# Kernel tuning notes

Measured on AMD Instinct MI355X. Metric: run time of the kernel, lower is better.

The kernel has to match this reference:

```python
import jax, jax.numpy as jnp
import numpy as np

NUM_HEADS = 8


def _conv1x1(x, W, b):
    # 1x1 conv == per-pixel linear: x [N,C,H,W], W [O,C], b [O]
    return jnp.einsum('nchw,oc->nohw', x, W) + b[None, :, None, None]


def setup_inputs() -> dict:
    key = jax.random.key(0)
    ks = jax.random.split(key, 10)
    C = 512
    s = 1.0 / np.sqrt(C)  # keep pre-softmax logits in a sane range
    return {
        'x': jax.random.normal(ks[0], (2, C, 64, 64), dtype=jnp.float32),
        'Wq': jax.random.normal(ks[1], (C, C), dtype=jnp.float32) * s,
        'bq': jax.random.normal(ks[2], (C,), dtype=jnp.float32) * 0.01,
        'Wk': jax.random.normal(ks[3], (C, C), dtype=jnp.float32) * s,
        'bk': jax.random.normal(ks[4], (C,), dtype=jnp.float32) * 0.01,
        'Wv': jax.random.normal(ks[5], (C, C), dtype=jnp.float32) * s,
        'bv': jax.random.normal(ks[6], (C,), dtype=jnp.float32) * 0.01,
        'Wo': jax.random.normal(ks[7], (C, C), dtype=jnp.float32) * s,
        'bo': jax.random.normal(ks[8], (C,), dtype=jnp.float32) * 0.01,
        'gamma': jax.random.normal(ks[9], (1,), dtype=jnp.float32),
    }


def reference(x, Wq, bq, Wk, bk, Wv, bv, Wo, bo, gamma):
    N, C, H, W = x.shape
    nh = NUM_HEADS
    hd = C // nh
    S = H * W
    scale = 1.0 / (hd ** 0.5)
    # Projections via 1x1 conv, then split heads over flattened spatial tokens
    Q = _conv1x1(x, Wq, bq).reshape(N, nh, hd, S).transpose(0, 1, 3, 2)  # [N,h,S,d]
    K = _conv1x1(x, Wk, bk).reshape(N, nh, hd, S)                         # [N,h,d,S]
    V = _conv1x1(x, Wv, bv).reshape(N, nh, hd, S).transpose(0, 1, 3, 2)  # [N,h,S,d]
    attn = jax.nn.softmax(jnp.einsum('nhsd,nhdt->nhst', Q, K) * scale, axis=-1)
    out = jnp.einsum('nhst,nhtd->nhsd', attn, V)                          # [N,h,S,d]
    out = out.transpose(0, 1, 3, 2).reshape(N, C, H, W)
    out = _conv1x1(out, Wo, bo)
    return gamma[0] * out + x
```

## Files before the change

### kernel.cpp

```cpp
#include <hip/hip_runtime.h>
#include <hip/hip_bf16.h>

typedef __attribute__((ext_vector_type(4))) float f32x4;
typedef __attribute__((ext_vector_type(16))) float f32x16;
typedef __attribute__((ext_vector_type(8))) short s16x8;
typedef __attribute__((ext_vector_type(4))) unsigned short us16x4;
typedef __attribute__((ext_vector_type(4))) unsigned int u32x4;

#define C_DIM 512
#define S_DIM 4096
#define NB 2
#define NH 8
#define HD 64

#define QSCALE 0.1803368801111244f

__device__ __forceinline__ unsigned short f2bf(float f) {
    union { float f; unsigned u; } v; v.f = f;
    unsigned r = v.u + 0x7FFFu + ((v.u >> 16) & 1u);
    return (unsigned short)(r >> 16);
}

__device__ __forceinline__ float dev_exp2(float x) {
    float r;
    asm("v_exp_f32 %0, %1" : "=v"(r) : "v"(x));
    return r;
}

__device__ __forceinline__ unsigned cvt_pk_bf16(float lo, float hi) {
    unsigned r;
    asm("v_cvt_pk_bf16_f32 %0, %1, %2" : "=v"(r) : "v"(lo), "v"(hi));
    return r;
}

__device__ __forceinline__ void lane_swap(unsigned& a, unsigned& b) {
    asm("v_permlane32_swap_b32 %0, %1" : "+v"(a), "+v"(b));
}

__global__ __launch_bounds__(256) void wconv_kernel(
    const float* __restrict__ Wq, const float* __restrict__ Wk,
    const float* __restrict__ Wv, const float* __restrict__ Wo,
    unsigned short* __restrict__ Wb) {
    int i = blockIdx.x * 256 + threadIdx.x;
    int y = blockIdx.y;
    const float* src = (y == 0) ? Wq : (y == 1) ? Wk : (y == 2) ? Wv : Wo;
    Wb[(size_t)y * 262144 + i] = f2bf(src[i]);
}

__global__ __launch_bounds__(256) void xpose_kernel(
    const float* __restrict__ x, unsigned short* __restrict__ Xt) {
    __shared__ float tile[32][33];
    int n = blockIdx.z;
    int s0 = blockIdx.x * 32;
    int c0 = blockIdx.y * 32;
    int tx = threadIdx.x & 31;
    int ty = threadIdx.x >> 5;
#pragma unroll
    for (int r = 0; r < 4; ++r) {
        int c = c0 + ty + r * 8;
        tile[ty + r * 8][tx] = x[((size_t)n * C_DIM + c) * S_DIM + s0 + tx];
    }
    __syncthreads();
#pragma unroll
    for (int r = 0; r < 4; ++r) {
        int s = s0 + ty + r * 8;
        Xt[((size_t)n * S_DIM + s) * C_DIM + c0 + tx] = f2bf(tile[tx][ty + r * 8]);
    }
}

__global__ __launch_bounds__(256) void qkv_gemm_kernel(
    const unsigned short* __restrict__ Wb, const unsigned short* __restrict__ Xt,
    const float* __restrict__ bq, const float* __restrict__ bk, const float* __restrict__ bv,
    unsigned short* __restrict__ Qt, unsigned short* __restrict__ Kt,
    unsigned short* __restrict__ Vb) {
    __shared__ unsigned short As[128 * 72];
    __shared__ unsigned short Bs[128 * 72];
    int w = blockIdx.z >> 1;
    int n = blockIdx.z & 1;
    const unsigned short* A = Wb + (size_t)w * 262144;
    const unsigned short* B = Xt + (size_t)n * S_DIM * C_DIM;
    int tid = threadIdx.x;
    int wid = tid >> 6, lane = tid & 63;
    int wm = wid >> 1, wn = wid & 1;
    int lr = lane & 15, lq = lane >> 4;
    int bm = blockIdx.y * 128, bt = blockIdx.x * 128;

    f32x4 zero = {0.f, 0.f, 0.f, 0.f};
    f32x4 acc[4][4];
#pragma unroll
    for (int i = 0; i < 4; ++i)
#pragma unroll
        for (int j = 0; j < 4; ++j) acc[i][j] = zero;

    for (int ks = 0; ks < 8; ++ks) {
#pragma unroll
        for (int q = 0; q < 4; ++q) {
            int cc = tid * 4 + q;
            int row = cc >> 3, col8 = (cc & 7) * 8;
            s16x8 av = *(const s16x8*)(A + (size_t)(bm + row) * C_DIM + ks * 64 + col8);
            *(s16x8*)&As[row * 72 + col8] = av;
            s16x8 bvv = *(const s16x8*)(B + (size_t)(bt + row) * C_DIM + ks * 64 + col8);
            *(s16x8*)&Bs[row * 72 + col8] = bvv;
        }
        __syncthreads();
#pragma unroll
        for (int kk = 0; kk < 2; ++kk) {
            s16x8 af[4], bf[4];
#pragma unroll
            for (int i = 0; i < 4; ++i)
                af[i] = *(const s16x8*)&As[(wm * 64 + i * 16 + lr) * 72 + kk * 32 + lq * 8];
#pragma unroll
            for (int j = 0; j < 4; ++j)
                bf[j] = *(const s16x8*)&Bs[(wn * 64 + j * 16 + lr) * 72 + kk * 32 + lq * 8];
#pragma unroll
            for (int i = 0; i < 4; ++i)
#pragma unroll
                for (int j = 0; j < 4; ++j)
                    acc[i][j] = __builtin_amdgcn_mfma_f32_16x16x32_bf16(af[i], bf[j], acc[i][j], 0, 0, 0);
        }
        __syncthreads();
    }

    const float* bias = (w == 0) ? bq : (w == 1) ? bk : bv;
#pragma unroll
    for (int i = 0; i < 4; ++i) {
        int obase = bm + wm * 64 + i * 16 + lq * 4;
#pragma unroll
        for (int j = 0; j < 4; ++j) {
            int t = bt + wn * 64 + j * 16 + lr;
            if (w == 0) {
                us16x4 pk;
#pragma unroll
                for (int r = 0; r < 4; ++r)
                    pk[r] = f2bf((acc[i][j][r] + bias[obase + r]) * QSCALE);
                int h = obase >> 6, d = obase & 63;
                *(us16x4*)&Qt[(((size_t)(n * NH + h) * S_DIM) + t) * HD + d] = pk;
            } else if (w == 1) {
                us16x4 pk;
#pragma unroll
                for (int r = 0; r < 4; ++r) pk[r] = f2bf(acc[i][j][r] + bias[obase + r]);
                int h = obase >> 6, d = obase & 63;
                *(us16x4*)&Kt[(((size_t)(n * NH + h) * S_DIM) + t) * HD + d] = pk;
            } else {
#pragma unroll
                for (int r = 0; r < 4; ++r) {
                    int o = obase + r;
                    Vb[((size_t)(n * C_DIM + o)) * S_DIM + t] = f2bf(acc[i][j][r] + bias[o]);
                }
            }
        }
    }
}

__global__ __launch_bounds__(256) void attn_kernel(
    const unsigned short* __restrict__ Qt, const unsigned short* __restrict__ Kt,
    const unsigned short* __restrict__ Vb, unsigned short* __restrict__ Ot) {
    __shared__ unsigned short Ks[64 * 64];
    __shared__ unsigned short Vs[64 * 64];
    int tid = threadIdx.x, wid = tid >> 6, lane = tid & 63;
    int l31 = lane & 31, hi = lane >> 5;

    int bidl = blockIdx.x;
    int swz = (bidl & 7) * 64 + (bidl >> 3);
    int nh = swz >> 5;
    int qb = swz & 31;
    int n = nh >> 3, h = nh & 7;
    int qrow0 = qb * 128 + wid * 32;

    const unsigned short* Qh = Qt + (size_t)nh * S_DIM * HD;
    const unsigned short* Kh = Kt + (size_t)nh * S_DIM * HD;
    const unsigned short* Vh = Vb + ((size_t)(n * C_DIM + h * HD)) * S_DIM;

    s16x8 qf[4];
#pragma unroll
    for (int s = 0; s < 4; ++s)
        qf[s] = *(const s16x8*)&Qh[((size_t)(qrow0 + l31)) * HD + s * 16 + hi * 8];

    s16x8 ones;
#pragma unroll
    for (int r = 0; r < 8; ++r) ones[r] = (short)0x3F80;

    f32x16 Oacc[2], Lacc;
#pragma unroll
    for (int jm = 0; jm < 2; ++jm)
#pragma unroll
        for (int r = 0; r < 16; ++r) Oacc[jm][r] = 0.f;
#pragma unroll
    for (int r = 0; r < 16; ++r) Lacc[r] = 0.f;

    int srow0 = tid >> 3, sslot = tid & 7;

    s16x8 kreg[2], vreg[2];
#pragma unroll
    for (int q = 0; q < 2; ++q) {
        int row = srow0 + q * 32;
        kreg[q] = *(const s16x8*)&Kh[((size_t)row) * HD + sslot * 8];
        vreg[q] = *(const s16x8*)&Vh[((size_t)row) * S_DIM + sslot * 8];
    }

    for (int kt = 0; kt < 64; ++kt) {
#pragma unroll
        for (int q = 0; q < 2; ++q) {
            int row = srow0 + q * 32;
            int ws = (sslot ^ (row & 7)) * 8;
            *(s16x8*)&Ks[row * 64 + ws] = kreg[q];
            *(s16x8*)&Vs[row * 64 + ws] = vreg[q];
        }
        __syncthreads();
        if (kt < 63) {
#pragma unroll
            for (int q = 0; q < 2; ++q) {
                int row = srow0 + q * 32;
                kreg[q] = *(const s16x8*)&Kh[((size_t)((kt + 1) * 64 + row)) * HD + sslot * 8];
                vreg[q] = *(const s16x8*)&Vh[((size_t)row) * S_DIM + (kt + 1) * 64 + sslot * 8];
            }
        }

        f32x16 s_[2];
#pragma unroll
        for (int jm = 0; jm < 2; ++jm) {
#pragma unroll
            for (int r = 0; r < 16; ++r) s_[jm][r] = 0.f;
            int arow = jm * 32 + l31;
            int sw = (arow & 7);
#pragma unroll
            for (int st = 0; st < 4; ++st) {
                s16x8 kf = *(const s16x8*)&Ks[arow * 64 + ((2 * st + hi) ^ sw) * 8];
                s_[jm] = __builtin_amdgcn_mfma_f32_32x32x16_bf16(kf, qf[st], s_[jm], 0, 0, 0);
            }
        }

        s16x8 pf[2][2];
#pragma unroll
        for (int jm = 0; jm < 2; ++jm) {
            unsigned pk0 = cvt_pk_bf16(dev_exp2(s_[jm][0]),  dev_exp2(s_[jm][1]));
            unsigned pk1 = cvt_pk_bf16(dev_exp2(s_[jm][2]),  dev_exp2(s_[jm][3]));
            unsigned pk2 = cvt_pk_bf16(dev_exp2(s_[jm][4]),  dev_exp2(s_[jm][5]));
            unsigned pk3 = cvt_pk_bf16(dev_exp2(s_[jm][6]),  dev_exp2(s_[jm][7]));
            unsigned pk4 = cvt_pk_bf16(dev_exp2(s_[jm][8]),  dev_exp2(s_[jm][9]));
            unsigned pk5 = cvt_pk_bf16(dev_exp2(s_[jm][10]), dev_exp2(s_[jm][11]));
            unsigned pk6 = cvt_pk_bf16(dev_exp2(s_[jm][12]), dev_exp2(s_[jm][13]));
            unsigned pk7 = cvt_pk_bf16(dev_exp2(s_[jm][14]), dev_exp2(s_[jm][15]));
            lane_swap(pk2, pk0);
            lane_swap(pk3, pk1);
            lane_swap(pk6, pk4);
            lane_swap(pk7, pk5);
            u32x4 w0 = {pk0, pk1, pk2, pk3};
            u32x4 w1 = {pk4, pk5, pk6, pk7};
            pf[jm][0] = __builtin_bit_cast(s16x8, w0);
            pf[jm][1] = __builtin_bit_cast(s16x8, w1);
        }

#pragma unroll
        for (int jm = 0; jm < 2; ++jm)
#pragma unroll
            for (int st = 0; st < 2; ++st)
                Lacc = __builtin_amdgcn_mfma_f32_32x32x16_bf16(ones, pf[jm][st], Lacc, 0, 0, 0);

#pragma unroll
        for (int jm2 = 0; jm2 < 2; ++jm2) {
            int vrow = jm2 * 32 + l31;
            int sw = (vrow & 7);
#pragma unroll
            for (int jm = 0; jm < 2; ++jm)
#pragma unroll
                for (int st = 0; st < 2; ++st) {
                    s16x8 vf = *(const s16x8*)&Vs[vrow * 64 + ((jm * 4 + st * 2 + hi) ^ sw) * 8];
                    Oacc[jm2] = __builtin_amdgcn_mfma_f32_32x32x16_bf16(vf, pf[jm][st], Oacc[jm2], 0, 0, 0);
                }
        }
        __syncthreads();
    }

    float inv = 1.f / Lacc[0];
    int token = qrow0 + l31;
    unsigned short* orow = Ot + ((size_t)n * S_DIM + token) * C_DIM + h * HD;
#pragma unroll
    for (int jm2 = 0; jm2 < 2; ++jm2)
#pragma unroll
        for (int rq = 0; rq < 4; ++rq) {
            int d = jm2 * 32 + 8 * rq + 4 * hi;
            us16x4 pk;
#pragma unroll
            for (int r = 0; r < 4; ++r) pk[r] = f2bf(Oacc[jm2][rq * 4 + r] * inv);
            *(us16x4*)&orow[d] = pk;
        }
}

__global__ __launch_bounds__(256) void out_gemm_kernel(
    const unsigned short* __restrict__ Wb, const unsigned short* __restrict__ Ot,
    const float* __restrict__ bo, const float* __restrict__ gamma,
    const float* __restrict__ xin, float* __restrict__ out) {
    __shared__ unsigned short As[128 * 72];
    __shared__ unsigned short Bs[128 * 72];
    int n = blockIdx.z;
    const unsigned short* A = Wb + (size_t)3 * 262144;
    const unsigned short* B = Ot + (size_t)n * S_DIM * C_DIM;
    int tid = threadIdx.x;
    int wid = tid >> 6, lane = tid & 63;
    int wm = wid >> 1, wn = wid & 1;
    int lr = lane & 15, lq = lane >> 4;
    int bm = blockIdx.y * 128, bt = blockIdx.x * 128;

    f32x4 zero = {0.f, 0.f, 0.f, 0.f};
    f32x4 acc[4][4];
#pragma unroll
    for (int i = 0; i < 4; ++i)
#pragma unroll
        for (int j = 0; j < 4; ++j) acc[i][j] = zero;

    for (int ks = 0; ks < 8; ++ks) {
#pragma unroll
        for (int q = 0; q < 4; ++q) {
            int cc = tid * 4 + q;
            int row = cc >> 3, col8 = (cc & 7) * 8;
            s16x8 av = *(const s16x8*)(A + (size_t)(bm + row) * C_DIM + ks * 64 + col8);
            *(s16x8*)&As[row * 72 + col8] = av;
            s16x8 bvv = *(const s16x8*)(B + (size_t)(bt + row) * C_DIM + ks * 64 + col8);
            *(s16x8*)&Bs[row * 72 + col8] = bvv;
        }
        __syncthreads();
#pragma unroll
        for (int kk = 0; kk < 2; ++kk) {
            s16x8 af[4], bf[4];
#pragma unroll
            for (int i = 0; i < 4; ++i)
                af[i] = *(const s16x8*)&As[(wm * 64 + i * 16 + lr) * 72 + kk * 32 + lq * 8];
#pragma unroll
            for (int j = 0; j < 4; ++j)
                bf[j] = *(const s16x8*)&Bs[(wn * 64 + j * 16 + lr) * 72 + kk * 32 + lq * 8];
#pragma unroll
            for (int i = 0; i < 4; ++i)
#pragma unroll
                for (int j = 0; j < 4; ++j)
                    acc[i][j] = __builtin_amdgcn_mfma_f32_16x16x32_bf16(af[i], bf[j], acc[i][j], 0, 0, 0);
        }
        __syncthreads();
    }

    float g = gamma[0];
#pragma unroll
    for (int i = 0; i < 4; ++i) {
        int obase = bm + wm * 64 + i * 16 + lq * 4;
#pragma unroll
        for (int j = 0; j < 4; ++j) {
            int t = bt + wn * 64 + j * 16 + lr;
#pragma unroll
            for (int r = 0; r < 4; ++r) {
                int o = obase + r;
                size_t idx = ((size_t)(n * C_DIM + o)) * S_DIM + t;
                out[idx] = g * (acc[i][j][r] + bo[o]) + xin[idx];
            }
        }
    }
}

extern "C" void kernel_launch(void* const* d_in, const int* in_sizes, int n_in,
                              void* d_out, int out_size, void* d_ws, size_t ws_size,
                              hipStream_t stream) {
    const float* x  = (const float*)d_in[0];
    const float* Wq = (const float*)d_in[1];
    const float* bq = (const float*)d_in[2];
    const float* Wk = (const float*)d_in[3];
    const float* bk = (const float*)d_in[4];
    const float* Wv = (const float*)d_in[5];
    const float* bv = (const float*)d_in[6];
    const float* Wo = (const float*)d_in[7];
    const float* bo = (const float*)d_in[8];
    const float* gamma = (const float*)d_in[9];
    float* out = (float*)d_out;

    char* ws = (char*)d_ws;
    unsigned short* Wb = (unsigned short*)ws;
    unsigned short* Xt = (unsigned short*)(ws + ((size_t)2  << 20));
    unsigned short* Qt = (unsigned short*)(ws + ((size_t)10 << 20));
    unsigned short* Kt = (unsigned short*)(ws + ((size_t)18 << 20));
    unsigned short* Vb = (unsigned short*)(ws + ((size_t)26 << 20));
    unsigned short* Ot = (unsigned short*)(ws + ((size_t)34 << 20));

    wconv_kernel<<<dim3(1024, 4), 256, 0, stream>>>(Wq, Wk, Wv, Wo, Wb);
    xpose_kernel<<<dim3(128, 16, 2), 256, 0, stream>>>(x, Xt);
    qkv_gemm_kernel<<<dim3(32, 4, 6), 256, 0, stream>>>(Wb, Xt, bq, bk, bv, Qt, Kt, Vb);
    attn_kernel<<<512, 256, 0, stream>>>(Qt, Kt, Vb, Ot);
    out_gemm_kernel<<<dim3(32, 4, 2), 256, 0, stream>>>(Wb, Ot, bo, gamma, x, out);
}
```

Measured before the change: 150.2 us.

## Double-buffer attention with 64 query rows per wave; use direct global-to-LDS loads in GEMMs

The attention kernel now gives each wave 64 query rows instead of 32, so each K/V fragment read from LDS is reused across two query sub-tiles. The grid is halved to 256 blocks, K/V go through double-buffered LDS with one barrier per tile, and the row sum is accumulated in VALU registers rather than through an MFMA against a ones vector. Both GEMM kernels load their tiles with global_load_lds straight into unpadded LDS, skipping the register round trip. In exchange, LDS reads in the GEMMs may now hit bank conflicts without the padding, and register pressure in attention rises, with only 256 blocks to fill the device.

```diff
diff --git a/kernel.cpp b/kernel.cpp
--- a/kernel.cpp
+++ b/kernel.cpp
@@ -35,6 +35,15 @@
 
 __device__ __forceinline__ void lane_swap(unsigned& a, unsigned& b) {
     asm("v_permlane32_swap_b32 %0, %1" : "+v"(a), "+v"(b));
+}
+__device__ __forceinline__ void lane_swapf(float& a, float& b) {
+    asm("v_permlane32_swap_b32 %0, %1" : "+v"(a), "+v"(b));
+}
+
+__device__ __forceinline__ void gload_lds16(const void* g, void* l) {
+    __builtin_amdgcn_global_load_lds(
+        (const __attribute__((address_space(1))) void*)g,
+        (__attribute__((address_space(3))) void*)l, 16, 0, 0);
 }
 
 __global__ __launch_bounds__(256) void wconv_kernel(
@@ -73,8 +82,8 @@
     const float* __restrict__ bq, const float* __restrict__ bk, const float* __restrict__ bv,
     unsigned short* __restrict__ Qt, unsigned short* __restrict__ Kt,
     unsigned short* __restrict__ Vb) {
-    __shared__ unsigned short As[128 * 72];
-    __shared__ unsigned short Bs[128 * 72];
+    __shared__ unsigned short As[128 * 64];
+    __shared__ unsigned short Bs[128 * 64];
     int w = blockIdx.z >> 1;
     int n = blockIdx.z & 1;
     const unsigned short* A = Wb + (size_t)w * 262144;
@@ -84,6 +93,7 @@
     int wm = wid >> 1, wn = wid & 1;
     int lr = lane & 15, lq = lane >> 4;
     int bm = blockIdx.y * 128, bt = blockIdx.x * 128;
+    int r_in = lane >> 3, c8 = (lane & 7) * 8;
 
     f32x4 zero = {0.f, 0.f, 0.f, 0.f};
     f32x4 acc[4][4];
@@ -95,12 +105,9 @@
     for (int ks = 0; ks < 8; ++ks) {
 #pragma unroll
         for (int q = 0; q < 4; ++q) {
-            int cc = tid * 4 + q;
-            int row = cc >> 3, col8 = (cc & 7) * 8;
-            s16x8 av = *(const s16x8*)(A + (size_t)(bm + row) * C_DIM + ks * 64 + col8);
-            *(s16x8*)&As[row * 72 + col8] = av;
-            s16x8 bvv = *(const s16x8*)(B + (size_t)(bt + row) * C_DIM + ks * 64 + col8);
-            *(s16x8*)&Bs[row * 72 + col8] = bvv;
+            int row = wid * 32 + q * 8;
+            gload_lds16(A + (size_t)(bm + row + r_in) * C_DIM + ks * 64 + c8, &As[row * 64]);
+            gload_lds16(B + (size_t)(bt + row + r_in) * C_DIM + ks * 64 + c8, &Bs[row * 64]);
         }
         __syncthreads();
 #pragma unroll
@@ -108,10 +115,10 @@
             s16x8 af[4], bf[4];
 #pragma unroll
             for (int i = 0; i < 4; ++i)
-                af[i] = *(const s16x8*)&As[(wm * 64 + i * 16 + lr) * 72 + kk * 32 + lq * 8];
+                af[i] = *(const s16x8*)&As[(wm * 64 + i * 16 + lr) * 64 + kk * 32 + lq * 8];
 #pragma unroll
             for (int j = 0; j < 4; ++j)
-                bf[j] = *(const s16x8*)&Bs[(wn * 64 + j * 16 + lr) * 72 + kk * 32 + lq * 8];
+                bf[j] = *(const s16x8*)&Bs[(wn * 64 + j * 16 + lr) * 64 + kk * 32 + lq * 8];
 #pragma unroll
             for (int i = 0; i < 4; ++i)
 #pragma unroll
@@ -152,43 +159,44 @@
     }
 }
 
-__global__ __launch_bounds__(256) void attn_kernel(
+__global__ __launch_bounds__(256, 1) void attn_kernel(
     const unsigned short* __restrict__ Qt, const unsigned short* __restrict__ Kt,
     const unsigned short* __restrict__ Vb, unsigned short* __restrict__ Ot) {
-    __shared__ unsigned short Ks[64 * 64];
-    __shared__ unsigned short Vs[64 * 64];
+    __shared__ unsigned short Ks[2][64 * 64];
+    __shared__ unsigned short Vs[2][64 * 64];
     int tid = threadIdx.x, wid = tid >> 6, lane = tid & 63;
     int l31 = lane & 31, hi = lane >> 5;
+    int sw = l31 & 7;
 
     int bidl = blockIdx.x;
-    int swz = (bidl & 7) * 64 + (bidl >> 3);
-    int nh = swz >> 5;
-    int qb = swz & 31;
+    int swz = (bidl & 7) * 32 + (bidl >> 3);
+    int nh = swz >> 4;
+    int qb = swz & 15;
     int n = nh >> 3, h = nh & 7;
-    int qrow0 = qb * 128 + wid * 32;
+    int qrow0 = qb * 256 + wid * 64;
 
     const unsigned short* Qh = Qt + (size_t)nh * S_DIM * HD;
     const unsigned short* Kh = Kt + (size_t)nh * S_DIM * HD;
     const unsigned short* Vh = Vb + ((size_t)(n * C_DIM + h * HD)) * S_DIM;
 
-    s16x8 qf[4];
-#pragma unroll
-    for (int s = 0; s < 4; ++s)
-        qf[s] = *(const s16x8*)&Qh[((size_t)(qrow0 + l31)) * HD + s * 16 + hi * 8];
-
-    s16x8 ones;
-#pragma unroll
-    for (int r = 0; r < 8; ++r) ones[r] = (short)0x3F80;
-
-    f32x16 Oacc[2], Lacc;
-#pragma unroll
-    for (int jm = 0; jm < 2; ++jm)
-#pragma unroll
-        for (int r = 0; r < 16; ++r) Oacc[jm][r] = 0.f;
-#pragma unroll
-    for (int r = 0; r < 16; ++r) Lacc[r] = 0.f;
+    s16x8 qf[2][4];
+#pragma unroll
+    for (int qs = 0; qs < 2; ++qs)
+#pragma unroll
+        for (int st = 0; st < 4; ++st)
+            qf[qs][st] = *(const s16x8*)&Qh[((size_t)(qrow0 + qs * 32 + l31)) * HD + st * 16 + hi * 8];
+
+    f32x16 Oacc[2][2];
+#pragma unroll
+    for (int qs = 0; qs < 2; ++qs)
+#pragma unroll
+        for (int jm = 0; jm < 2; ++jm)
+#pragma unroll
+            for (int r = 0; r < 16; ++r) Oacc[qs][jm][r] = 0.f;
+    float l_run[2] = {0.f, 0.f};
 
     int srow0 = tid >> 3, sslot = tid & 7;
+    int ws0 = (sslot ^ (srow0 & 7)) * 8;
 
     s16x8 kreg[2], vreg[2];
 #pragma unroll
@@ -197,16 +205,16 @@
         kreg[q] = *(const s16x8*)&Kh[((size_t)row) * HD + sslot * 8];
         vreg[q] = *(const s16x8*)&Vh[((size_t)row) * S_DIM + sslot * 8];
     }
+#pragma unroll
+    for (int q = 0; q < 2; ++q) {
+        int row = srow0 + q * 32;
+        *(s16x8*)&Ks[0][row * 64 + ws0] = kreg[q];
+        *(s16x8*)&Vs[0][row * 64 + ws0] = vreg[q];
+    }
+    __syncthreads();
 
     for (int kt = 0; kt < 64; ++kt) {
-#pragma unroll
-        for (int q = 0; q < 2; ++q) {
-            int row = srow0 + q * 32;
-            int ws = (sslot ^ (row & 7)) * 8;
-            *(s16x8*)&Ks[row * 64 + ws] = kreg[q];
-            *(s16x8*)&Vs[row * 64 + ws] = vreg[q];
-        }
-        __syncthreads();
+        int cur = kt & 1;
         if (kt < 63) {
 #pragma unroll
             for (int q = 0; q < 2; ++q) {
@@ -216,83 +224,102 @@
             }
         }
 
-        f32x16 s_[2];
-#pragma unroll
-        for (int jm = 0; jm < 2; ++jm) {
-#pragma unroll
-            for (int r = 0; r < 16; ++r) s_[jm][r] = 0.f;
-            int arow = jm * 32 + l31;
-            int sw = (arow & 7);
-#pragma unroll
-            for (int st = 0; st < 4; ++st) {
-                s16x8 kf = *(const s16x8*)&Ks[arow * 64 + ((2 * st + hi) ^ sw) * 8];
-                s_[jm] = __builtin_amdgcn_mfma_f32_32x32x16_bf16(kf, qf[st], s_[jm], 0, 0, 0);
-            }
-        }
-
-        s16x8 pf[2][2];
-#pragma unroll
-        for (int jm = 0; jm < 2; ++jm) {
-            unsigned pk0 = cvt_pk_bf16(dev_exp2(s_[jm][0]),  dev_exp2(s_[jm][1]));
-            unsigned pk1 = cvt_pk_bf16(dev_exp2(s_[jm][2]),  dev_exp2(s_[jm][3]));
-            unsigned pk2 = cvt_pk_bf16(dev_exp2(s_[jm][4]),  dev_exp2(s_[jm][5]));
-            unsigned pk3 = cvt_pk_bf16(dev_exp2(s_[jm][6]),  dev_exp2(s_[jm][7]));
-            unsigned pk4 = cvt_pk_bf16(dev_exp2(s_[jm][8]),  dev_exp2(s_[jm][9]));
-            unsigned pk5 = cvt_pk_bf16(dev_exp2(s_[jm][10]), dev_exp2(s_[jm][11]));
-            unsigned pk6 = cvt_pk_bf16(dev_exp2(s_[jm][12]), dev_exp2(s_[jm][13]));
-            unsigned pk7 = cvt_pk_bf16(dev_exp2(s_[jm][14]), dev_exp2(s_[jm][15]));
-            lane_swap(pk2, pk0);
-            lane_swap(pk3, pk1);
-            lane_swap(pk6, pk4);
-            lane_swap(pk7, pk5);
-            u32x4 w0 = {pk0, pk1, pk2, pk3};
-            u32x4 w1 = {pk4, pk5, pk6, pk7};
-            pf[jm][0] = __builtin_bit_cast(s16x8, w0);
-            pf[jm][1] = __builtin_bit_cast(s16x8, w1);
-        }
-
-#pragma unroll
-        for (int jm = 0; jm < 2; ++jm)
-#pragma unroll
-            for (int st = 0; st < 2; ++st)
-                Lacc = __builtin_amdgcn_mfma_f32_32x32x16_bf16(ones, pf[jm][st], Lacc, 0, 0, 0);
-
-#pragma unroll
-        for (int jm2 = 0; jm2 < 2; ++jm2) {
-            int vrow = jm2 * 32 + l31;
-            int sw = (vrow & 7);
+        f32x16 s_[2][2];
+#pragma unroll
+        for (int qs = 0; qs < 2; ++qs)
 #pragma unroll
             for (int jm = 0; jm < 2; ++jm)
 #pragma unroll
-                for (int st = 0; st < 2; ++st) {
-                    s16x8 vf = *(const s16x8*)&Vs[vrow * 64 + ((jm * 4 + st * 2 + hi) ^ sw) * 8];
-                    Oacc[jm2] = __builtin_amdgcn_mfma_f32_32x32x16_bf16(vf, pf[jm][st], Oacc[jm2], 0, 0, 0);
-                }
-        }
-        __syncthreads();
-    }
-
-    float inv = 1.f / Lacc[0];
-    int token = qrow0 + l31;
-    unsigned short* orow = Ot + ((size_t)n * S_DIM + token) * C_DIM + h * HD;
-#pragma unroll
-    for (int jm2 = 0; jm2 < 2; ++jm2)
-#pragma unroll
-        for (int rq = 0; rq < 4; ++rq) {
-            int d = jm2 * 32 + 8 * rq + 4 * hi;
-            us16x4 pk;
-#pragma unroll
-            for (int r = 0; r < 4; ++r) pk[r] = f2bf(Oacc[jm2][rq * 4 + r] * inv);
-            *(us16x4*)&orow[d] = pk;
-        }
+                for (int r = 0; r < 16; ++r) s_[qs][jm][r] = 0.f;
+#pragma unroll
+        for (int st = 0; st < 4; ++st) {
+            int slot = ((2 * st + hi) ^ sw) * 8;
+            s16x8 kf0 = *(const s16x8*)&Ks[cur][l31 * 64 + slot];
+            s16x8 kf1 = *(const s16x8*)&Ks[cur][(32 + l31) * 64 + slot];
+            s_[0][0] = __builtin_amdgcn_mfma_f32_32x32x16_bf16(kf0, qf[0][st], s_[0][0], 0, 0, 0);
+            s_[1][0] = __builtin_amdgcn_mfma_f32_32x32x16_bf16(kf0, qf[1][st], s_[1][0], 0, 0, 0);
+            s_[0][1] = __builtin_amdgcn_mfma_f32_32x32x16_bf16(kf1, qf[0][st], s_[0][1], 0, 0, 0);
+            s_[1][1] = __builtin_amdgcn_mfma_f32_32x32x16_bf16(kf1, qf[1][st], s_[1][1], 0, 0, 0);
+        }
+
+        s16x8 pf[2][4];
+#pragma unroll
+        for (int qs = 0; qs < 2; ++qs) {
+            float rs = 0.f;
+#pragma unroll
+            for (int jm = 0; jm < 2; ++jm) {
+                float p[16];
+#pragma unroll
+                for (int r = 0; r < 16; ++r) { p[r] = dev_exp2(s_[qs][jm][r]); rs += p[r]; }
+                unsigned pk0 = cvt_pk_bf16(p[0],  p[1]);
+                unsigned pk1 = cvt_pk_bf16(p[2],  p[3]);
+                unsigned pk2 = cvt_pk_bf16(p[4],  p[5]);
+                unsigned pk3 = cvt_pk_bf16(p[6],  p[7]);
+                unsigned pk4 = cvt_pk_bf16(p[8],  p[9]);
+                unsigned pk5 = cvt_pk_bf16(p[10], p[11]);
+                unsigned pk6 = cvt_pk_bf16(p[12], p[13]);
+                unsigned pk7 = cvt_pk_bf16(p[14], p[15]);
+                lane_swap(pk2, pk0);
+                lane_swap(pk3, pk1);
+                lane_swap(pk6, pk4);
+                lane_swap(pk7, pk5);
+                u32x4 w0 = {pk0, pk1, pk2, pk3};
+                u32x4 w1 = {pk4, pk5, pk6, pk7};
+                pf[qs][2 * jm]     = __builtin_bit_cast(s16x8, w0);
+                pf[qs][2 * jm + 1] = __builtin_bit_cast(s16x8, w1);
+            }
+            l_run[qs] += rs;
+        }
+
+#pragma unroll
+        for (int kk = 0; kk < 4; ++kk) {
+            int slot = ((kk * 2 + hi) ^ sw) * 8;
+            s16x8 vf0 = *(const s16x8*)&Vs[cur][l31 * 64 + slot];
+            s16x8 vf1 = *(const s16x8*)&Vs[cur][(32 + l31) * 64 + slot];
+            Oacc[0][0] = __builtin_amdgcn_mfma_f32_32x32x16_bf16(vf0, pf[0][kk], Oacc[0][0], 0, 0, 0);
+            Oacc[1][0] = __builtin_amdgcn_mfma_f32_32x32x16_bf16(vf0, pf[1][kk], Oacc[1][0], 0, 0, 0);
+            Oacc[0][1] = __builtin_amdgcn_mfma_f32_32x32x16_bf16(vf1, pf[0][kk], Oacc[0][1], 0, 0, 0);
+            Oacc[1][1] = __builtin_amdgcn_mfma_f32_32x32x16_bf16(vf1, pf[1][kk], Oacc[1][1], 0, 0, 0);
+        }
+
+        if (kt < 63) {
+            int nxt = cur ^ 1;
+#pragma unroll
+            for (int q = 0; q < 2; ++q) {
+                int row = srow0 + q * 32;
+                *(s16x8*)&Ks[nxt][row * 64 + ws0] = kreg[q];
+                *(s16x8*)&Vs[nxt][row * 64 + ws0] = vreg[q];
+            }
+            __syncthreads();
+        }
+    }
+
+#pragma unroll
+    for (int qs = 0; qs < 2; ++qs) {
+        float a = l_run[qs], b = l_run[qs];
+        lane_swapf(a, b);
+        float inv = 1.f / (a + b);
+        int token = qrow0 + qs * 32 + l31;
+        unsigned short* orow = Ot + ((size_t)n * S_DIM + token) * C_DIM + h * HD;
+#pragma unroll
+        for (int jm2 = 0; jm2 < 2; ++jm2)
+#pragma unroll
+            for (int rq = 0; rq < 4; ++rq) {
+                int d = jm2 * 32 + 8 * rq + 4 * hi;
+                us16x4 pk;
+#pragma unroll
+                for (int r = 0; r < 4; ++r) pk[r] = f2bf(Oacc[qs][jm2][rq * 4 + r] * inv);
+                *(us16x4*)&orow[d] = pk;
+            }
+    }
 }
 
 __global__ __launch_bounds__(256) void out_gemm_kernel(
     const unsigned short* __restrict__ Wb, const unsigned short* __restrict__ Ot,
     const float* __restrict__ bo, const float* __restrict__ gamma,
     const float* __restrict__ xin, float* __restrict__ out) {
-    __shared__ unsigned short As[128 * 72];
-    __shared__ unsigned short Bs[128 * 72];
+    __shared__ unsigned short As[128 * 64];
+    __shared__ unsigned short Bs[128 * 64];
     int n = blockIdx.z;
     const unsigned short* A = Wb + (size_t)3 * 262144;
     const unsigned short* B = Ot + (size_t)n * S_DIM * C_DIM;
@@ -301,6 +328,7 @@
     int wm = wid >> 1, wn = wid & 1;
     int lr = lane & 15, lq = lane >> 4;
     int bm = blockIdx.y * 128, bt = blockIdx.x * 128;
+    int r_in = lane >> 3, c8 = (lane & 7) * 8;
 
     f32x4 zero = {0.f, 0.f, 0.f, 0.f};
     f32x4 acc[4][4];
@@ -312,12 +340,9 @@
     for (int ks = 0; ks < 8; ++ks) {
 #pragma unroll
         for (int q = 0; q < 4; ++q) {
-            int cc = tid * 4 + q;
-            int row = cc >> 3, col8 = (cc & 7) * 8;
-            s16x8 av = *(const s16x8*)(A + (size_t)(bm + row) * C_DIM + ks * 64 + col8);
-            *(s16x8*)&As[row * 72 + col8] = av;
-            s16x8 bvv = *(const s16x8*)(B + (size_t)(bt + row) * C_DIM + ks * 64 + col8);
-            *(s16x8*)&Bs[row * 72 + col8] = bvv;
+            int row = wid * 32 + q * 8;
+            gload_lds16(A + (size_t)(bm + row + r_in) * C_DIM + ks * 64 + c8, &As[row * 64]);
+            gload_lds16(B + (size_t)(bt + row + r_in) * C_DIM + ks * 64 + c8, &Bs[row * 64]);
         }
         __syncthreads();
 #pragma unroll
@@ -325,10 +350,10 @@
             s16x8 af[4], bf[4];
 #pragma unroll
             for (int i = 0; i < 4; ++i)
-                af[i] = *(const s16x8*)&As[(wm * 64 + i * 16 + lr) * 72 + kk * 32 + lq * 8];
+                af[i] = *(const s16x8*)&As[(wm * 64 + i * 16 + lr) * 64 + kk * 32 + lq * 8];
 #pragma unroll
             for (int j = 0; j < 4; ++j)
-                bf[j] = *(const s16x8*)&Bs[(wn * 64 + j * 16 + lr) * 72 + kk * 32 + lq * 8];
+                bf[j] = *(const s16x8*)&Bs[(wn * 64 + j * 16 + lr) * 64 + kk * 32 + lq * 8];
 #pragma unroll
             for (int i = 0; i < 4; ++i)
 #pragma unroll
@@ -381,6 +406,6 @@
     wconv_kernel<<<dim3(1024, 4), 256, 0, stream>>>(Wq, Wk, Wv, Wo, Wb);
     xpose_kernel<<<dim3(128, 16, 2), 256, 0, stream>>>(x, Xt);
     qkv_gemm_kernel<<<dim3(32, 4, 6), 256, 0, stream>>>(Wb, Xt, bq, bk, bv, Qt, Kt, Vb);
-    attn_kernel<<<512, 256, 0, stream>>>(Qt, Kt, Vb, Ot);
+    attn_kernel<<<256, 256, 0, stream>>>(Qt, Kt, Vb, Ot);
     out_gemm_kernel<<<dim3(32, 4, 2), 256, 0, stream>>>(Wb, Ot, bo, gamma, x, out);
 }
```

Measured after the change: 155.5 us. +3.5%, slower.
